# Kernel tuning notes

Measured on AMD Instinct MI355X. Metric: run time of the kernel, lower is better.

Reference implementation:

```python
import jax, jax.numpy as jnp
import numpy as np

N_NODES = 100000
N_EDGES = 2000000
F_IN = 32
HID = 32
N_CLASS = 40


def _gru_cell(m, h, wih, whh, bih, bhh):
    # torch.nn.GRUCell math; wih/whh: [3H, H_in], gates ordered r, z, n
    gi = m @ wih.T + bih
    gh = h @ whh.T + bhh
    i_r, i_z, i_n = jnp.split(gi, 3, axis=-1)
    h_r, h_z, h_n = jnp.split(gh, 3, axis=-1)
    r = jax.nn.sigmoid(i_r + h_r)
    z = jax.nn.sigmoid(i_z + h_z)
    n = jnp.tanh(i_n + r * h_n)
    return (1.0 - z) * n + z * h


def _gated_conv(x, edge_index, edge_weight, w_proj, w_msg, wih, whh, bih, bhh):
    h = x @ w_proj                                   # [N, out]
    msg = (h @ w_msg)[edge_index[0]] * edge_weight[:, None]  # gather src -> [E, out]
    agg = jax.ops.segment_sum(msg, edge_index[1], num_segments=N_NODES)  # scatter-add to dst
    return _gru_cell(agg, h, wih, whh, bih, bhh)


def setup_inputs() -> dict:
    key = jax.random.key(0)
    ks = jax.random.split(key, 16)
    s = 0.1
    return {
        "x": jax.random.normal(ks[0], (N_NODES, F_IN), jnp.float32),
        "edge_index": jax.random.randint(ks[1], (2, N_EDGES), 0, N_NODES, jnp.int64),
        "edge_weight": jax.random.uniform(ks[2], (N_EDGES,), jnp.float32),
        "W1_proj": jax.random.normal(ks[3], (F_IN, HID), jnp.float32) * s,
        "W1_msg": jax.random.normal(ks[4], (HID, HID), jnp.float32) * s,
        "gru1_wih": jax.random.normal(ks[5], (3 * HID, HID), jnp.float32) * s,
        "gru1_whh": jax.random.normal(ks[6], (3 * HID, HID), jnp.float32) * s,
        "gru1_bih": jax.random.normal(ks[7], (3 * HID,), jnp.float32) * s,
        "gru1_bhh": jax.random.normal(ks[8], (3 * HID,), jnp.float32) * s,
        "W2_proj": jax.random.normal(ks[9], (HID, N_CLASS), jnp.float32) * s,
        "W2_msg": jax.random.normal(ks[10], (N_CLASS, N_CLASS), jnp.float32) * s,
        "gru2_wih": jax.random.normal(ks[11], (3 * N_CLASS, N_CLASS), jnp.float32) * s,
        "gru2_whh": jax.random.normal(ks[12], (3 * N_CLASS, N_CLASS), jnp.float32) * s,
        "gru2_bih": jax.random.normal(ks[13], (3 * N_CLASS,), jnp.float32) * s,
        "gru2_bhh": jax.random.normal(ks[14], (3 * N_CLASS,), jnp.float32) * s,
    }


def reference(x, edge_index, edge_weight, W1_proj, W1_msg, gru1_wih, gru1_whh,
              gru1_bih, gru1_bhh, W2_proj, W2_msg, gru2_wih, gru2_whh,
              gru2_bih, gru2_bhh):
    # eval mode: dropout is identity
    h = _gated_conv(x, edge_index, edge_weight, W1_proj, W1_msg,
                    gru1_wih, gru1_whh, gru1_bih, gru1_bhh)
    h = jax.nn.relu(h)
    h = _gated_conv(h, edge_index, edge_weight, W2_proj, W2_msg,
                    gru2_wih, gru2_whh, gru2_bih, gru2_bhh)
    return jax.nn.log_softmax(h, axis=-1)
```

## Files before the change

kernel.cpp:

```cpp
#include <hip/hip_runtime.h>
#include <math.h>

#define NN 100000
#define NP 100032
#define NE 2000000
#define FIN 32
#define H 32
#define NC 40

#define NBK 196
#define BSH 9
#define CAP 10880
#define NSL 4
#define EPT 16
#define EPB (256 * EPT)

typedef _Float16 half_t;
typedef __attribute__((ext_vector_type(8))) _Float16 half8;
typedef __attribute__((ext_vector_type(4))) _Float16 half4;
typedef __attribute__((ext_vector_type(4))) float f32x4;
typedef long long ll2 __attribute__((ext_vector_type(2)));

__device__ __forceinline__ float sigm_(float x) {
    return 1.0f / (1.0f + __expf(-x));
}
__device__ __forceinline__ float tanh_(float x) {
    x = fminf(fmaxf(x, -20.0f), 20.0f);
    float e = __expf(2.0f * x);
    return (e - 1.0f) / (e + 1.0f);
}

__global__ __launch_bounds__(256) void kA_bucket(const int* __restrict__ ei,
                                                 const float* __restrict__ ew,
                                                 int* __restrict__ gcur,
                                                 long long* __restrict__ rec) {
    __shared__ long long recs[EPB];
    __shared__ int gdst[EPB];
    __shared__ int cnt[NBK], base[NBK], sofs[NBK];
    __shared__ int ssc[256];
    int tid = threadIdx.x;
    for (int i = tid; i < NBK; i += 256) cnt[i] = 0;
    __syncthreads();
    int e0 = blockIdx.x * EPB;
    int dcache[EPT];
#pragma unroll
    for (int i = 0; i < EPT; ++i) {
        int e = e0 + i * 256 + tid;
        dcache[i] = (e < NE) ? ei[NE + e] : -1;
        if (e < NE) atomicAdd(&cnt[dcache[i] >> BSH], 1);
    }
    __syncthreads();
    int cv = (tid < NBK) ? cnt[tid] : 0;
    ssc[tid] = cv;
    __syncthreads();
    for (int off = 1; off < 256; off <<= 1) {
        int v = (tid >= off) ? ssc[tid - off] : 0;
        __syncthreads();
        ssc[tid] += v;
        __syncthreads();
    }
    if (tid < NBK) {
        sofs[tid] = ssc[tid] - cv;
        base[tid] = atomicAdd(&gcur[tid], cv);
        cnt[tid] = 0;
    }
    __syncthreads();
#pragma unroll
    for (int i = 0; i < EPT; ++i) {
        int e = e0 + i * 256 + tid;
        if (e < NE) {
            int d = dcache[i], s = ei[e];
            int b = d >> BSH;
            int r = atomicAdd(&cnt[b], 1);
            int slot = sofs[b] + r;
            int pos = base[b] + r;
            int lo = s | ((d & 511) << 17);
            recs[slot] = (long long)(unsigned)lo |
                         ((long long)__float_as_int(ew[e]) << 32);
            gdst[slot] = (pos < CAP) ? (b * CAP + pos) : -1;
        }
    }
    __syncthreads();
    int nrec = min(EPB, NE - e0);
    for (int i = tid; i < nrec; i += 256) {
        int gd = gdst[i];
        if (gd >= 0) rec[gd] = recs[i];
    }
}

__global__ __launch_bounds__(256) void kB_sort(const int* __restrict__ gcur,
                                               const int2* __restrict__ rec,
                                               int2* __restrict__ evs,
                                               int* __restrict__ ofs2,
                                               int* __restrict__ cnt4) {
    __shared__ int hist[2048], lofs[2048], ssc[256];
    int tid = threadIdx.x, b = blockIdx.x;
    int nb0 = b << BSH;
    int nnodes = min(512, NN - nb0);
    int cntb = min(gcur[b], CAP);
    for (int i = tid; i < 2048; i += 256) hist[i] = 0;
    __syncthreads();
    const int2* rb = rec + (size_t)b * CAP;
    for (int i = tid; i < cntb; i += 256) {
        int rx = rb[i].x;
        int bin = (((rx & 0x1FFFF) >> 15) << BSH) | ((rx >> 17) & 511);
        atomicAdd(&hist[bin], 1);
    }
    __syncthreads();
    int base = tid * 8, ls = 0, lh[8];
#pragma unroll
    for (int j = 0; j < 8; ++j) {
        lh[j] = hist[base + j];
        ls += lh[j];
    }
    ssc[tid] = ls;
    __syncthreads();
    for (int off = 1; off < 256; off <<= 1) {
        int v = (tid >= off) ? ssc[tid - off] : 0;
        __syncthreads();
        ssc[tid] += v;
        __syncthreads();
    }
    int ex = ssc[tid] - ls;
#pragma unroll
    for (int j = 0; j < 8; ++j) {
        lofs[base + j] = ex;
        ex += lh[j];
    }
    __syncthreads();
    for (int l = tid; l < nnodes; l += 256) {
        int c0 = hist[l], c1 = hist[512 + l], c2 = hist[1024 + l], c3 = hist[1536 + l];
        cnt4[nb0 + l] = c0 | (c1 << 8) | (c2 << 16) | (c3 << 24);
        ofs2[0 * NN + nb0 + l] = b * CAP + lofs[l];
        ofs2[1 * NN + nb0 + l] = b * CAP + lofs[512 + l];
        ofs2[2 * NN + nb0 + l] = b * CAP + lofs[1024 + l];
        ofs2[3 * NN + nb0 + l] = b * CAP + lofs[1536 + l];
    }
    __syncthreads();
    for (int i = tid; i < 2048; i += 256) hist[i] = 0;
    __syncthreads();
    int2* eb = evs + (size_t)b * CAP;
    for (int i = tid; i < cntb; i += 256) {
        int2 r = rb[i];
        int bin = (((r.x & 0x1FFFF) >> 15) << BSH) | ((r.x >> 17) & 511);
        int rk = atomicAdd(&hist[bin], 1);
        eb[lofs[bin] + rk] = make_int2(r.x & 0x1FFFF, r.y);
    }
}

__global__ __launch_bounds__(256) void k_wpre(const float* __restrict__ W2m,
                                              const float* __restrict__ wih2,
                                              float* __restrict__ M2,
                                              int* __restrict__ gcur) {
    int i = blockIdx.x * 256 + threadIdx.x;
    if (i < NBK) gcur[i] = 0;
    if (i >= NC * 3 * NC) return;
    int u = i / (3 * NC), col = i % (3 * NC);
    float acc = 0.f;
#pragma unroll
    for (int t = 0; t < NC; ++t) acc += W2m[u * NC + t] * wih2[col * NC + t];
    M2[i] = acc;
}

__global__ __launch_bounds__(256) void k_wc(const float* __restrict__ W1m,
                                            const float* __restrict__ wih1,
                                            const float* __restrict__ W2p,
                                            const float* __restrict__ M2,
                                            const float* __restrict__ whh1,
                                            const float* __restrict__ whh2,
                                            half_t* __restrict__ W1sw,
                                            half_t* __restrict__ W2sw) {
    int i = blockIdx.x * 256 + threadIdx.x;
    if (i < 8192) {
        int j = i & 7, lane = (i >> 3) & 63, ct = (i >> 9) & 7, s = i >> 12;
        int k = s * 32 + (lane >> 4) * 8 + j;
        int col = ct * 16 + (lane & 15);
        int g = col >> 5, jj = col & 31;
        float v = 0.f;
        if (g <= 2) {
            if (k < 32) {
                float acc = 0.f;
#pragma unroll
                for (int t = 0; t < H; ++t) acc += W1m[k * H + t] * wih1[(g * H + jj) * H + t];
                v = acc;
            } else if (g < 2) {
                v = whh1[(g * H + jj) * H + (k - 32)];
            }
        } else {
            if (k >= 32) v = whh1[(2 * H + jj) * H + (k - 32)];
        }
        W1sw[i] = (half_t)v;
    } else if (i < 8192 + 18432) {
        int i2 = i - 8192;
        int j = i2 & 7, lane = (i2 >> 3) & 63;
        int tt = i2 >> 9;
        int ct = tt % 12, s = tt / 12;
        int k = s * 32 + (lane >> 4) * 8 + j;
        int col = ct * 16 + (lane & 15);
        int g = col / 48, jj = col % 48;
        float v = 0.f;
        if (jj < NC) {
            if (g <= 2) {
                if (k < 32) {
                    float acc = 0.f;
#pragma unroll
                    for (int u = 0; u < NC; ++u)
                        acc += W2p[k * NC + u] * M2[u * 3 * NC + g * NC + jj];
                    v = acc;
                } else if (k < 72 && g < 2) {
                    v = whh2[(g * NC + jj) * NC + (k - 32)];
                }
            } else {
                if (k >= 32 && k < 72) v = whh2[(2 * NC + jj) * NC + (k - 32)];
            }
        }
        W2sw[i2] = (half_t)v;
    }
}

__global__ __launch_bounds__(256) void k1_proj(const float* __restrict__ x,
                                               const float* __restrict__ Wp,
                                               half_t* __restrict__ Xc1,
                                               half_t* __restrict__ Hd) {
    __shared__ float sWp[FIN * H];
    __shared__ float sx[8][FIN];
    int tid = threadIdx.x;
    for (int i = tid; i < FIN * H; i += 256) sWp[i] = Wp[i];
    int nb = blockIdx.x * 8;
    int nl = tid >> 5, j = tid & 31;
    int n = nb + nl;
    if (n < NN) sx[nl][j] = x[(size_t)n * FIN + j];
    __syncthreads();
    float acc = 0.f;
#pragma unroll
    for (int k = 0; k < FIN; ++k) acc += sx[nl][k] * sWp[k * H + j];
    if (n < NN) {
        half_t hv = (half_t)acc;
        Xc1[(size_t)n * 64 + 32 + j] = hv;
        Hd[(size_t)n * 32 + j] = hv;
    }
}

__global__ __launch_bounds__(320) void k4_proj2(const half_t* __restrict__ Hh,
                                                const float* __restrict__ Wp,
                                                half_t* __restrict__ Xc2) {
    __shared__ float sWp[FIN * NC];
    __shared__ float shn[8][FIN];
    int tid = threadIdx.x;
    for (int i = tid; i < FIN * NC; i += 320) sWp[i] = Wp[i];
    int nb = blockIdx.x * 8;
    if (tid < 256) {
        int r = tid >> 5, c = tid & 31;
        shn[r][c] = (float)Hh[(size_t)(nb + r) * 32 + c];
    }
    if (tid < 192) {
        int r = tid / 24, c = tid % 24;
        Xc2[(size_t)(nb + r) * 96 + 72 + c] = (half_t)0.f;
    }
    __syncthreads();
    int nl = tid / NC, j = tid % NC;
    int n = nb + nl;
    float acc = 0.f;
#pragma unroll
    for (int k = 0; k < FIN; ++k) acc += shn[nl][k] * sWp[k * NC + j];
    if (n < NN) Xc2[(size_t)n * 96 + 32 + j] = (half_t)acc;
}

template <int DSTR>
__global__ __launch_bounds__(256) void k_aggh(const int* __restrict__ ofs2,
                                              const int* __restrict__ cnt4,
                                              const int2* __restrict__ evs,
                                              const half_t* __restrict__ src,
                                              half_t* __restrict__ dst) {
    int idx = blockIdx.x * 256 + threadIdx.x;
    int n = idx >> 2, q = idx & 3;
    if (n >= NN) return;
    const half8* s8 = (const half8*)src + q;
    const long long* ev8 = (const long long*)evs;
    int cw = cnt4[n];
    float acc[8] = {0.f, 0.f, 0.f, 0.f, 0.f, 0.f, 0.f, 0.f};
#pragma unroll
    for (int s = 0; s < NSL; ++s) {
        int s0 = ofs2[s * NN + n];
        int c = (cw >> (8 * s)) & 255;
        int e = s0, e1 = s0 + c;
        if ((e & 1) && e < e1) {
            long long r = __builtin_nontemporal_load(ev8 + e);
            float w = __int_as_float((int)(r >> 32));
            half8 hv = s8[(size_t)(r & 0x1FFFF) * 4];
#pragma unroll
            for (int t = 0; t < 8; ++t) acc[t] += w * (float)hv[t];
            ++e;
        }
        for (; e + 4 <= e1; e += 4) {
            ll2 p0 = __builtin_nontemporal_load((const ll2*)(ev8 + e));
            ll2 p1 = __builtin_nontemporal_load((const ll2*)(ev8 + e + 2));
            half8 h0 = s8[(size_t)(p0[0] & 0x1FFFF) * 4];
            half8 h1 = s8[(size_t)(p0[1] & 0x1FFFF) * 4];
            half8 h2 = s8[(size_t)(p1[0] & 0x1FFFF) * 4];
            half8 h3 = s8[(size_t)(p1[1] & 0x1FFFF) * 4];
            float w0 = __int_as_float((int)(p0[0] >> 32));
            float w1 = __int_as_float((int)(p0[1] >> 32));
            float w2 = __int_as_float((int)(p1[0] >> 32));
            float w3 = __int_as_float((int)(p1[1] >> 32));
#pragma unroll
            for (int t = 0; t < 8; ++t) {
                acc[t] += w0 * (float)h0[t];
                acc[t] += w1 * (float)h1[t];
                acc[t] += w2 * (float)h2[t];
                acc[t] += w3 * (float)h3[t];
            }
        }
        if (e + 2 <= e1) {
            ll2 p0 = __builtin_nontemporal_load((const ll2*)(ev8 + e));
            half8 h0 = s8[(size_t)(p0[0] & 0x1FFFF) * 4];
            half8 h1 = s8[(size_t)(p0[1] & 0x1FFFF) * 4];
            float w0 = __int_as_float((int)(p0[0] >> 32));
            float w1 = __int_as_float((int)(p0[1] >> 32));
#pragma unroll
            for (int t = 0; t < 8; ++t) {
                acc[t] += w0 * (float)h0[t];
                acc[t] += w1 * (float)h1[t];
            }
            e += 2;
        }
        if (e < e1) {
            long long r = __builtin_nontemporal_load(ev8 + e);
            float w = __int_as_float((int)(r >> 32));
            half8 hv = s8[(size_t)(r & 0x1FFFF) * 4];
#pragma unroll
            for (int t = 0; t < 8; ++t) acc[t] += w * (float)hv[t];
        }
    }
    half8 o;
#pragma unroll
    for (int t = 0; t < 8; ++t) o[t] = (half_t)acc[t];
    *(half8*)(dst + (size_t)n * DSTR + q * 8) = o;
}

__global__ __launch_bounds__(256) void k3m(const half_t* __restrict__ Xc1,
                                           const half8* __restrict__ W1sw,
                                           const float* __restrict__ bih,
                                           const float* __restrict__ bhh,
                                           half_t* __restrict__ Hh) {
    int tid = threadIdx.x;
    int wave = tid >> 6, lane = tid & 63;
    int m16 = lane & 15, q = lane >> 4;
    int nb = blockIdx.x * 64 + wave * 16;
    const half8* xr = (const half8*)(Xc1 + (size_t)(nb + m16) * 64);
    half8 a0 = xr[q];
    half8 a1 = xr[4 + q];
    f32x4 acc[8];
#pragma unroll
    for (int ct = 0; ct < 8; ++ct) acc[ct] = (f32x4){0.f, 0.f, 0.f, 0.f};
#pragma unroll
    for (int ct = 0; ct < 8; ++ct) {
        acc[ct] = __builtin_amdgcn_mfma_f32_16x16x32_f16(a0, W1sw[ct * 64 + lane], acc[ct], 0, 0, 0);
        acc[ct] = __builtin_amdgcn_mfma_f32_16x16x32_f16(a1, W1sw[(8 + ct) * 64 + lane], acc[ct], 0, 0, 0);
    }
#pragma unroll
    for (int ct = 0; ct < 2; ++ct) {
        int j = ct * 16 + m16;
        float br = bih[j] + bhh[j];
        float bz = bih[H + j] + bhh[H + j];
        float bi = bih[2 * H + j], bh = bhh[2 * H + j];
#pragma unroll
        for (int m = 0; m < 4; ++m) {
            int node = nb + q * 4 + m;
            float r = sigm_(acc[ct][m] + br);
            float z = sigm_(acc[2 + ct][m] + bz);
            float ng = tanh_(acc[4 + ct][m] + bi + r * (acc[6 + ct][m] + bh));
            float hj = (float)Xc1[(size_t)node * 64 + 32 + j];
            float o = fmaxf((1.f - z) * ng + z * hj, 0.f);
            if (node < NN) Hh[(size_t)node * 32 + j] = (half_t)o;
        }
    }
}

__global__ __launch_bounds__(256) void k6m(const half_t* __restrict__ Xc2,
                                           const half8* __restrict__ W2sw,
                                           const float* __restrict__ bih,
                                           const float* __restrict__ bhh,
                                           float* __restrict__ out) {
    int tid = threadIdx.x;
    int wave = tid >> 6, lane = tid & 63;
    int m16 = lane & 15, q = lane >> 4;
    int nb = blockIdx.x * 64 + wave * 16;
    const half8* xr = (const half8*)(Xc2 + (size_t)(nb + m16) * 96);
    half8 a0 = xr[q], a1 = xr[4 + q], a2 = xr[8 + q];
    f32x4 acc[12];
#pragma unroll
    for (int ct = 0; ct < 12; ++ct) acc[ct] = (f32x4){0.f, 0.f, 0.f, 0.f};
#pragma unroll
    for (int ct = 0; ct < 12; ++ct) {
        acc[ct] = __builtin_amdgcn_mfma_f32_16x16x32_f16(a0, W2sw[ct * 64 + lane], acc[ct], 0, 0, 0);
        acc[ct] = __builtin_amdgcn_mfma_f32_16x16x32_f16(a1, W2sw[(12 + ct) * 64 + lane], acc[ct], 0, 0, 0);
        acc[ct] = __builtin_amdgcn_mfma_f32_16x16x32_f16(a2, W2sw[(24 + ct) * 64 + lane], acc[ct], 0, 0, 0);
    }
    float v[3][4];
#pragma unroll
    for (int ct = 0; ct < 3; ++ct) {
        int j = ct * 16 + m16;
        int jc = (j < NC) ? j : (NC - 1);
        float br = bih[jc] + bhh[jc];
        float bz = bih[NC + jc] + bhh[NC + jc];
        float bi = bih[2 * NC + jc], bh = bhh[2 * NC + jc];
#pragma unroll
        for (int m = 0; m < 4; ++m) {
            int node = nb + q * 4 + m;
            float r = sigm_(acc[ct][m] + br);
            float z = sigm_(acc[3 + ct][m] + bz);
            float ng = tanh_(acc[6 + ct][m] + bi + r * (acc[9 + ct][m] + bh));
            float hj = (float)Xc2[(size_t)node * 96 + 32 + jc];
            v[ct][m] = (1.f - z) * ng + z * hj;
        }
    }
    bool v2ok = (m16 < 8);
#pragma unroll
    for (int m = 0; m < 4; ++m) {
        float mx = fmaxf(v[0][m], v[1][m]);
        if (v2ok) mx = fmaxf(mx, v[2][m]);
#pragma unroll
        for (int d = 1; d < 16; d <<= 1) mx = fmaxf(mx, __shfl_xor(mx, d));
        float se = __expf(v[0][m] - mx) + __expf(v[1][m] - mx) +
                   (v2ok ? __expf(v[2][m] - mx) : 0.f);
#pragma unroll
        for (int d = 1; d < 16; d <<= 1) se += __shfl_xor(se, d);
        float ls = mx + __logf(se);
        int node = nb + q * 4 + m;
        if (node < NN) {
            out[(size_t)node * NC + m16] = v[0][m] - ls;
            out[(size_t)node * NC + 16 + m16] = v[1][m] - ls;
            if (v2ok) out[(size_t)node * NC + 32 + m16] = v[2][m] - ls;
        }
    }
}

extern "C" void kernel_launch(void* const* d_in, const int* in_sizes, int n_in,
                              void* d_out, int out_size, void* d_ws, size_t ws_size,
                              hipStream_t stream) {
    const float* x = (const float*)d_in[0];
    const int* ei = (const int*)d_in[1];
    const float* ew = (const float*)d_in[2];
    const float* W1p = (const float*)d_in[3];
    const float* W1m = (const float*)d_in[4];
    const float* g1wih = (const float*)d_in[5];
    const float* g1whh = (const float*)d_in[6];
    const float* g1bih = (const float*)d_in[7];
    const float* g1bhh = (const float*)d_in[8];
    const float* W2p = (const float*)d_in[9];
    const float* W2m = (const float*)d_in[10];
    const float* g2wih = (const float*)d_in[11];
    const float* g2whh = (const float*)d_in[12];
    const float* g2bih = (const float*)d_in[13];
    const float* g2bhh = (const float*)d_in[14];
    float* ws = (float*)d_ws;

    half_t* Xc = (half_t*)ws;
    half_t* Hd = (half_t*)(ws + 3201024);
    half_t* Hh = (half_t*)(ws + 4801536);
    int2* rec = (int2*)ws;
    int2* evs = (int2*)(ws + 6402048);
    int* ofs2 = (int*)(ws + 10667008);
    int* cnt4 = (int*)(ws + 11067008);
    int* gcur = (int*)(ws + 11167008);
    half_t* W1sw = (half_t*)(ws + 11167264);
    half_t* W2sw = W1sw + 8192;
    float* M2 = ws + 11180576;
    float* out = (float*)d_out;

    k_wpre<<<(NC * 3 * NC + 255) / 256, 256, 0, stream>>>(W2m, g2wih, M2, gcur);
    kA_bucket<<<(NE + EPB - 1) / EPB, 256, 0, stream>>>(ei, ew, gcur, (long long*)rec);
    kB_sort<<<NBK, 256, 0, stream>>>(gcur, rec, evs, ofs2, cnt4);
    k_wc<<<(8192 + 18432 + 255) / 256, 256, 0, stream>>>(
        W1m, g1wih, W2p, M2, g1whh, g2whh, W1sw, W2sw);

    k1_proj<<<NN / 8, 256, 0, stream>>>(x, W1p, Xc, Hd);
    k_aggh<64><<<(NN * 4 + 255) / 256, 256, 0, stream>>>(ofs2, cnt4, evs, Hd, Xc);
    k3m<<<NP / 64, 256, 0, stream>>>(Xc, (const half8*)W1sw, g1bih, g1bhh, Hh);

    k4_proj2<<<NN / 8, 320, 0, stream>>>(Hh, W2p, Xc);
    k_aggh<96><<<(NN * 4 + 255) / 256, 256, 0, stream>>>(ofs2, cnt4, evs, Hh, Xc);
    k6m<<<NP / 64, 256, 0, stream>>>(Xc, (const half8*)W2sw, g2bih, g2bhh, out);
}
```

Baseline: 298.4 us.

## Sort edges node-major so each destination has one contiguous edge segment

Changes the bin order in the bucket sort from source-slice-major to destination-node-major, so all edges of a destination node become one contiguous run. The aggregation kernel then reads a single offset and count per node instead of four slices, and unrolls the gather loop to 8 edges for more memory-level parallelism. Edges within a node are no longer grouped by source range across nodes, which may reduce L2 locality of the source-feature gathers. It also trades four small loops per node for one longer loop with fewer branch tails.

```diff
diff --git a/kernel.cpp b/kernel.cpp
--- a/kernel.cpp
+++ b/kernel.cpp
@@ -11,7 +11,6 @@
 #define NBK 196
 #define BSH 9
 #define CAP 10880
-#define NSL 4
 #define EPT 16
 #define EPB (256 * EPT)
 
@@ -91,8 +90,8 @@
 __global__ __launch_bounds__(256) void kB_sort(const int* __restrict__ gcur,
                                                const int2* __restrict__ rec,
                                                int2* __restrict__ evs,
-                                               int* __restrict__ ofs2,
-                                               int* __restrict__ cnt4) {
+                                               int* __restrict__ ofs,
+                                               int* __restrict__ ocn) {
     __shared__ int hist[2048], lofs[2048], ssc[256];
     int tid = threadIdx.x, b = blockIdx.x;
     int nb0 = b << BSH;
@@ -103,7 +102,7 @@
     const int2* rb = rec + (size_t)b * CAP;
     for (int i = tid; i < cntb; i += 256) {
         int rx = rb[i].x;
-        int bin = (((rx & 0x1FFFF) >> 15) << BSH) | ((rx >> 17) & 511);
+        int bin = (((rx >> 17) & 511) << 2) | ((rx & 0x1FFFF) >> 15);
         atomicAdd(&hist[bin], 1);
     }
     __syncthreads();
@@ -129,12 +128,9 @@
     }
     __syncthreads();
     for (int l = tid; l < nnodes; l += 256) {
-        int c0 = hist[l], c1 = hist[512 + l], c2 = hist[1024 + l], c3 = hist[1536 + l];
-        cnt4[nb0 + l] = c0 | (c1 << 8) | (c2 << 16) | (c3 << 24);
-        ofs2[0 * NN + nb0 + l] = b * CAP + lofs[l];
-        ofs2[1 * NN + nb0 + l] = b * CAP + lofs[512 + l];
-        ofs2[2 * NN + nb0 + l] = b * CAP + lofs[1024 + l];
-        ofs2[3 * NN + nb0 + l] = b * CAP + lofs[1536 + l];
+        int c = hist[4 * l] + hist[4 * l + 1] + hist[4 * l + 2] + hist[4 * l + 3];
+        ofs[nb0 + l] = b * CAP + lofs[4 * l];
+        ocn[nb0 + l] = c;
     }
     __syncthreads();
     for (int i = tid; i < 2048; i += 256) hist[i] = 0;
@@ -142,7 +138,7 @@
     int2* eb = evs + (size_t)b * CAP;
     for (int i = tid; i < cntb; i += 256) {
         int2 r = rb[i];
-        int bin = (((r.x & 0x1FFFF) >> 15) << BSH) | ((r.x >> 17) & 511);
+        int bin = (((r.x >> 17) & 511) << 2) | ((r.x & 0x1FFFF) >> 15);
         int rk = atomicAdd(&hist[bin], 1);
         eb[lofs[bin] + rk] = make_int2(r.x & 0x1FFFF, r.y);
     }
@@ -267,8 +263,8 @@
 }
 
 template <int DSTR>
-__global__ __launch_bounds__(256) void k_aggh(const int* __restrict__ ofs2,
-                                              const int* __restrict__ cnt4,
+__global__ __launch_bounds__(256) void k_aggh(const int* __restrict__ ofs,
+                                              const int* __restrict__ ocn,
                                               const int2* __restrict__ evs,
                                               const half_t* __restrict__ src,
                                               half_t* __restrict__ dst) {
@@ -277,60 +273,89 @@
     if (n >= NN) return;
     const half8* s8 = (const half8*)src + q;
     const long long* ev8 = (const long long*)evs;
-    int cw = cnt4[n];
+    int e = ofs[n];
+    int e1 = e + ocn[n];
     float acc[8] = {0.f, 0.f, 0.f, 0.f, 0.f, 0.f, 0.f, 0.f};
-#pragma unroll
-    for (int s = 0; s < NSL; ++s) {
-        int s0 = ofs2[s * NN + n];
-        int c = (cw >> (8 * s)) & 255;
-        int e = s0, e1 = s0 + c;
-        if ((e & 1) && e < e1) {
-            long long r = __builtin_nontemporal_load(ev8 + e);
-            float w = __int_as_float((int)(r >> 32));
-            half8 hv = s8[(size_t)(r & 0x1FFFF) * 4];
-#pragma unroll
-            for (int t = 0; t < 8; ++t) acc[t] += w * (float)hv[t];
-            ++e;
-        }
-        for (; e + 4 <= e1; e += 4) {
-            ll2 p0 = __builtin_nontemporal_load((const ll2*)(ev8 + e));
-            ll2 p1 = __builtin_nontemporal_load((const ll2*)(ev8 + e + 2));
-            half8 h0 = s8[(size_t)(p0[0] & 0x1FFFF) * 4];
-            half8 h1 = s8[(size_t)(p0[1] & 0x1FFFF) * 4];
-            half8 h2 = s8[(size_t)(p1[0] & 0x1FFFF) * 4];
-            half8 h3 = s8[(size_t)(p1[1] & 0x1FFFF) * 4];
-            float w0 = __int_as_float((int)(p0[0] >> 32));
-            float w1 = __int_as_float((int)(p0[1] >> 32));
-            float w2 = __int_as_float((int)(p1[0] >> 32));
-            float w3 = __int_as_float((int)(p1[1] >> 32));
-#pragma unroll
-            for (int t = 0; t < 8; ++t) {
-                acc[t] += w0 * (float)h0[t];
-                acc[t] += w1 * (float)h1[t];
-                acc[t] += w2 * (float)h2[t];
-                acc[t] += w3 * (float)h3[t];
-            }
-        }
-        if (e + 2 <= e1) {
-            ll2 p0 = __builtin_nontemporal_load((const ll2*)(ev8 + e));
-            half8 h0 = s8[(size_t)(p0[0] & 0x1FFFF) * 4];
-            half8 h1 = s8[(size_t)(p0[1] & 0x1FFFF) * 4];
-            float w0 = __int_as_float((int)(p0[0] >> 32));
-            float w1 = __int_as_float((int)(p0[1] >> 32));
-#pragma unroll
-            for (int t = 0; t < 8; ++t) {
-                acc[t] += w0 * (float)h0[t];
-                acc[t] += w1 * (float)h1[t];
-            }
-            e += 2;
-        }
-        if (e < e1) {
-            long long r = __builtin_nontemporal_load(ev8 + e);
-            float w = __int_as_float((int)(r >> 32));
-            half8 hv = s8[(size_t)(r & 0x1FFFF) * 4];
-#pragma unroll
-            for (int t = 0; t < 8; ++t) acc[t] += w * (float)hv[t];
-        }
+    if ((e & 1) && e < e1) {
+        long long r = __builtin_nontemporal_load(ev8 + e);
+        float w = __int_as_float((int)(r >> 32));
+        half8 hv = s8[(size_t)(r & 0x1FFFF) * 4];
+#pragma unroll
+        for (int t = 0; t < 8; ++t) acc[t] += w * (float)hv[t];
+        ++e;
+    }
+    for (; e + 8 <= e1; e += 8) {
+        ll2 p0 = __builtin_nontemporal_load((const ll2*)(ev8 + e));
+        ll2 p1 = __builtin_nontemporal_load((const ll2*)(ev8 + e + 2));
+        ll2 p2 = __builtin_nontemporal_load((const ll2*)(ev8 + e + 4));
+        ll2 p3 = __builtin_nontemporal_load((const ll2*)(ev8 + e + 6));
+        half8 h0 = s8[(size_t)(p0[0] & 0x1FFFF) * 4];
+        half8 h1 = s8[(size_t)(p0[1] & 0x1FFFF) * 4];
+        half8 h2 = s8[(size_t)(p1[0] & 0x1FFFF) * 4];
+        half8 h3 = s8[(size_t)(p1[1] & 0x1FFFF) * 4];
+        half8 h4 = s8[(size_t)(p2[0] & 0x1FFFF) * 4];
+        half8 h5 = s8[(size_t)(p2[1] & 0x1FFFF) * 4];
+        half8 h6 = s8[(size_t)(p3[0] & 0x1FFFF) * 4];
+        half8 h7 = s8[(size_t)(p3[1] & 0x1FFFF) * 4];
+        float w0 = __int_as_float((int)(p0[0] >> 32));
+        float w1 = __int_as_float((int)(p0[1] >> 32));
+        float w2 = __int_as_float((int)(p1[0] >> 32));
+        float w3 = __int_as_float((int)(p1[1] >> 32));
+        float w4 = __int_as_float((int)(p2[0] >> 32));
+        float w5 = __int_as_float((int)(p2[1] >> 32));
+        float w6 = __int_as_float((int)(p3[0] >> 32));
+        float w7 = __int_as_float((int)(p3[1] >> 32));
+#pragma unroll
+        for (int t = 0; t < 8; ++t) {
+            acc[t] += w0 * (float)h0[t];
+            acc[t] += w1 * (float)h1[t];
+            acc[t] += w2 * (float)h2[t];
+            acc[t] += w3 * (float)h3[t];
+            acc[t] += w4 * (float)h4[t];
+            acc[t] += w5 * (float)h5[t];
+            acc[t] += w6 * (float)h6[t];
+            acc[t] += w7 * (float)h7[t];
+        }
+    }
+    if (e + 4 <= e1) {
+        ll2 p0 = __builtin_nontemporal_load((const ll2*)(ev8 + e));
+        ll2 p1 = __builtin_nontemporal_load((const ll2*)(ev8 + e + 2));
+        half8 h0 = s8[(size_t)(p0[0] & 0x1FFFF) * 4];
+        half8 h1 = s8[(size_t)(p0[1] & 0x1FFFF) * 4];
+        half8 h2 = s8[(size_t)(p1[0] & 0x1FFFF) * 4];
+        half8 h3 = s8[(size_t)(p1[1] & 0x1FFFF) * 4];
+        float w0 = __int_as_float((int)(p0[0] >> 32));
+        float w1 = __int_as_float((int)(p0[1] >> 32));
+        float w2 = __int_as_float((int)(p1[0] >> 32));
+        float w3 = __int_as_float((int)(p1[1] >> 32));
+#pragma unroll
+        for (int t = 0; t < 8; ++t) {
+            acc[t] += w0 * (float)h0[t];
+            acc[t] += w1 * (float)h1[t];
+            acc[t] += w2 * (float)h2[t];
+            acc[t] += w3 * (float)h3[t];
+        }
+        e += 4;
+    }
+    if (e + 2 <= e1) {
+        ll2 p0 = __builtin_nontemporal_load((const ll2*)(ev8 + e));
+        half8 h0 = s8[(size_t)(p0[0] & 0x1FFFF) * 4];
+        half8 h1 = s8[(size_t)(p0[1] & 0x1FFFF) * 4];
+        float w0 = __int_as_float((int)(p0[0] >> 32));
+        float w1 = __int_as_float((int)(p0[1] >> 32));
+#pragma unroll
+        for (int t = 0; t < 8; ++t) {
+            acc[t] += w0 * (float)h0[t];
+            acc[t] += w1 * (float)h1[t];
+        }
+        e += 2;
+    }
+    if (e < e1) {
+        long long r = __builtin_nontemporal_load(ev8 + e);
+        float w = __int_as_float((int)(r >> 32));
+        half8 hv = s8[(size_t)(r & 0x1FFFF) * 4];
+#pragma unroll
+        for (int t = 0; t < 8; ++t) acc[t] += w * (float)hv[t];
     }
     half8 o;
 #pragma unroll
@@ -461,25 +486,25 @@
     half_t* Hh = (half_t*)(ws + 4801536);
     int2* rec = (int2*)ws;
     int2* evs = (int2*)(ws + 6402048);
-    int* ofs2 = (int*)(ws + 10667008);
-    int* cnt4 = (int*)(ws + 11067008);
-    int* gcur = (int*)(ws + 11167008);
-    half_t* W1sw = (half_t*)(ws + 11167264);
+    int* ofs = (int*)(ws + 10667008);
+    int* ocn = (int*)(ws + 10767008);
+    int* gcur = (int*)(ws + 10867008);
+    half_t* W1sw = (half_t*)(ws + 10867264);
     half_t* W2sw = W1sw + 8192;
-    float* M2 = ws + 11180576;
+    float* M2 = ws + 10880576;
     float* out = (float*)d_out;
 
     k_wpre<<<(NC * 3 * NC + 255) / 256, 256, 0, stream>>>(W2m, g2wih, M2, gcur);
     kA_bucket<<<(NE + EPB - 1) / EPB, 256, 0, stream>>>(ei, ew, gcur, (long long*)rec);
-    kB_sort<<<NBK, 256, 0, stream>>>(gcur, rec, evs, ofs2, cnt4);
+    kB_sort<<<NBK, 256, 0, stream>>>(gcur, rec, evs, ofs, ocn);
     k_wc<<<(8192 + 18432 + 255) / 256, 256, 0, stream>>>(
         W1m, g1wih, W2p, M2, g1whh, g2whh, W1sw, W2sw);
 
     k1_proj<<<NN / 8, 256, 0, stream>>>(x, W1p, Xc, Hd);
-    k_aggh<64><<<(NN * 4 + 255) / 256, 256, 0, stream>>>(ofs2, cnt4, evs, Hd, Xc);
+    k_aggh<64><<<(NN * 4 + 255) / 256, 256, 0, stream>>>(ofs, ocn, evs, Hd, Xc);
     k3m<<<NP / 64, 256, 0, stream>>>(Xc, (const half8*)W1sw, g1bih, g1bhh, Hh);
 
     k4_proj2<<<NN / 8, 320, 0, stream>>>(Hh, W2p, Xc);
-    k_aggh<96><<<(NN * 4 + 255) / 256, 256, 0, stream>>>(ofs2, cnt4, evs, Hh, Xc);
+    k_aggh<96><<<(NN * 4 + 255) / 256, 256, 0, stream>>>(ofs, ocn, evs, Hh, Xc);
     k6m<<<NP / 64, 256, 0, stream>>>(Xc, (const half8*)W2sw, g2bih, g2bhh, out);
 }
```

After: 303.7 us. About the same (+1.8%).
